# Optimization experiments

Hardware: AMD Instinct MI355X
Metric: run time of the kernel (lower is better)

The kernel has to match this reference:

```python
import jax, jax.numpy as jnp
import numpy as np

REF_SCALE = 5.0


def _forward_warp(im, flow):
    """Bilinear scatter-add (splat) forward warp.
    im: [B,C,H,W], flow: [B,H,W,2] in pixel units. Returns [B,C,H,W].
    A pixel contributes to its 4 bilinear neighbors only if the whole
    2x2 footprint is inside the image (matches the CUDA kernel).
    """
    B, C, H, W = im.shape
    xs = flow[..., 0] + jnp.arange(W, dtype=flow.dtype)            # [B,H,W]
    ys = flow[..., 1] + jnp.arange(H, dtype=flow.dtype)[:, None]   # [B,H,W]
    x0 = jnp.floor(xs); y0 = jnp.floor(ys)
    x1 = x0 + 1.0;      y1 = y0 + 1.0
    valid = (x0 >= 0) & (x1 <= W - 1) & (y0 >= 0) & (y1 <= H - 1)
    x0i = x0.astype(jnp.int32); y0i = y0.astype(jnp.int32)
    x1i = x1.astype(jnp.int32); y1i = y1.astype(jnp.int32)
    w_nw = (x1 - xs) * (y1 - ys)
    w_ne = (xs - x0) * (y1 - ys)
    w_sw = (x1 - xs) * (ys - y0)
    w_se = (xs - x0) * (ys - y0)

    def splat_one(im_b, idx_b, w_b):
        # im_b: [C,H,W], idx_b: [H,W] int32, w_b: [H,W]
        contrib = (im_b * w_b).reshape(C, -1).T                    # [HW, C]
        return jax.ops.segment_sum(contrib, idx_b.reshape(-1), num_segments=H * W)

    out = jnp.zeros((B, H * W, C), dtype=im.dtype)
    for w_c, yi, xi in ((w_nw, y0i, x0i), (w_ne, y0i, x1i),
                        (w_sw, y1i, x0i), (w_se, y1i, x1i)):
        idx = jnp.where(valid, yi * W + xi, 0)
        wv = jnp.where(valid, w_c, jnp.zeros_like(w_c))
        out = out + jax.vmap(splat_one)(im, idx, wv)
    return out.transpose(0, 2, 1).reshape(B, C, H, W)


def setup_inputs() -> dict:
    key = jax.random.key(0)
    k1, k2, k3 = jax.random.split(key, 3)
    B, C, H, W = 8, 3, 384, 1280
    x = jax.random.normal(k1, (B, C, H, W), dtype=jnp.float32)
    flow = jax.random.normal(k2, (B, 2, H, W), dtype=jnp.float32) * 20.0  # realistic px displacement
    depth = jax.random.uniform(k3, (B, 1, H, W), dtype=jnp.float32) * 80.0  # metric depth [0,80]
    return {"x": x, "flow": flow, "depth": depth}


def reference(x, flow, depth):
    B, C, H, W = x.shape
    flow = jnp.clip(flow, -2.0 * W, 2.0 * W)
    flow = jnp.transpose(flow, (0, 2, 3, 1))                       # [B,H,W,2]
    depth = jnp.clip(depth, 0.001, 80.0)
    depth_weight = jnp.exp(-(depth - 40.0) / REF_SCALE)            # [B,1,H,W]
    mask = jnp.ones_like(depth)
    # Fuse the three splats (depth_weight, x*depth_weight, mask) into one
    # warp over stacked channels -- identical math, one scatter pass.
    stacked = jnp.concatenate([depth_weight, x * depth_weight, mask], axis=1)  # [B, 1+C+1, H, W]
    warped = _forward_warp(stacked, flow)
    dw_flowed = warped[:, 0:1]
    xw_flowed = warped[:, 1:1 + C]
    mask_flowed = warped[:, 1 + C:2 + C]
    invalid = mask_flowed < 0.5                                    # [B,1,H,W]
    xw_flowed = jnp.where(invalid, jnp.zeros_like(xw_flowed), xw_flowed)
    return xw_flowed / jnp.maximum(dw_flowed, 1e-7)
```

## Files before the change

kernel.cpp:

```cpp
#include <hip/hip_runtime.h>
#include <hip/hip_fp16.h>
#include <math.h>

#define BB 8
#define CC 3
#define HH 384
#define WW 1280
#define HW (HH * WW)
#define NPIX (BB * HW)

#define TILE 32
#define TXN 40
#define TYN 12
#define TILES (TXN * TYN)
#define BINS (BB * TILES)

#define PPT 16
#define TPB 256
#define PPB (PPT * TPB)
#define NBLK ((NPIX + PPB - 1) / PPB)


#define HPAD 1280
#define CAPL 2048
#define RCH 8
#define LCAP 1280

__device__ __forceinline__ int enc_of(int idx, const float* __restrict__ flow) {
  int b = idx / HW;
  int p = idx - b * HW;
  int h = p / WW;
  int w = p - h * WW;
  float fx = flow[(b * 2 + 0) * HW + p];
  float fy = flow[(b * 2 + 1) * HW + p];
  fx = fminf(fmaxf(fx, -2560.0f), 2560.0f);
  fy = fminf(fmaxf(fy, -2560.0f), 2560.0f);
  float xs = fx + (float)w;
  float ys = fy + (float)h;
  float x0 = floorf(xs);
  float y0 = floorf(ys);
  if (!(x0 >= 0.0f && x0 <= (float)(WW - 2) && y0 >= 0.0f &&
        y0 <= (float)(HH - 2)))
    return -1;
  int x0i = (int)x0;
  int y0i = (int)y0;
  int enc = (b * TILES + (y0i >> 5) * TXN + (x0i >> 5));
  if ((x0i & 31) == 31) enc |= 1 << 22;
  if ((y0i & 31) == 31) enc |= 1 << 23;
  return enc;
}

__device__ inline void splat_direct(int b, int p, const float* __restrict__ x,
                                    const float* __restrict__ flow,
                                    const float* __restrict__ depth,
                                    float* __restrict__ xw_acc,
                                    float* __restrict__ dw_acc,
                                    float* __restrict__ mask_acc) {
  int h = p / WW;
  int w = p - h * WW;
  float fx = flow[(b * 2 + 0) * HW + p];
  float fy = flow[(b * 2 + 1) * HW + p];
  fx = fminf(fmaxf(fx, -2560.0f), 2560.0f);
  fy = fminf(fmaxf(fy, -2560.0f), 2560.0f);
  float xs = fx + (float)w;
  float ys = fy + (float)h;
  float x0 = floorf(xs);
  float y0 = floorf(ys);
  if (!(x0 >= 0.0f && x0 <= (float)(WW - 2) && y0 >= 0.0f &&
        y0 <= (float)(HH - 2)))
    return;
  int x0i = (int)x0;
  int y0i = (int)y0;
  float ax = xs - x0;
  float ay = ys - y0;
  float w_nw = (1.0f - ax) * (1.0f - ay);
  float w_ne = ax * (1.0f - ay);
  float w_sw = (1.0f - ax) * ay;
  float w_se = ax * ay;
  float d = depth[b * HW + p];
  d = fminf(fmaxf(d, 0.001f), 80.0f);
  float dw = expf(-(d - 40.0f) * 0.2f);
  float xv0 = x[(b * CC + 0) * HW + p] * dw;
  float xv1 = x[(b * CC + 1) * HW + p] * dw;
  float xv2 = x[(b * CC + 2) * HW + p] * dw;
  float* dwb = dw_acc + b * HW;
  float* mkb = mask_acc + b * HW;
  float* xb0 = xw_acc + (b * CC + 0) * HW;
  float* xb1 = xw_acc + (b * CC + 1) * HW;
  float* xb2 = xw_acc + (b * CC + 2) * HW;
  int i_nw = y0i * WW + x0i;
  int ci[4] = {i_nw, i_nw + 1, i_nw + WW, i_nw + WW + 1};
  float cw[4] = {w_nw, w_ne, w_sw, w_se};
  for (int c = 0; c < 4; ++c) {
    atomicAdd(dwb + ci[c], cw[c] * dw);
    atomicAdd(mkb + ci[c], cw[c]);
    atomicAdd(xb0 + ci[c], cw[c] * xv0);
    atomicAdd(xb1 + ci[c], cw[c] * xv1);
    atomicAdd(xb2 + ci[c], cw[c] * xv2);
  }
}

__global__ __launch_bounds__(256) void splat_kernel(
    const float* __restrict__ x, const float* __restrict__ flow,
    const float* __restrict__ depth, float* __restrict__ xw_acc,
    float* __restrict__ dw_acc, float* __restrict__ mask_acc) {
  int idx = blockIdx.x * blockDim.x + threadIdx.x;
  if (idx >= NPIX) return;
  int b = idx / HW;
  int p = idx - b * HW;
  splat_direct(b, p, x, flow, depth, xw_acc, dw_acc, mask_acc);
}

__global__ __launch_bounds__(256) void normalize_kernel(
    float* __restrict__ out, const float* __restrict__ dw_acc,
    const float* __restrict__ mask_acc) {
  int idx = blockIdx.x * blockDim.x + threadIdx.x;
  if (idx >= NPIX) return;
  int b = idx / HW;
  int p = idx - b * HW;
  float m = mask_acc[b * HW + p];
  float dwv = dw_acc[b * HW + p];
  float inv = 1.0f / fmaxf(dwv, 1e-7f);
  bool invalid = (m < 0.5f);
  float* ob = out + (b * CC) * HW + p;
  for (int c = 0; c < CC; ++c) {
    float xw = ob[c * HW];
    ob[c * HW] = invalid ? 0.0f : xw * inv;
  }
}

__global__ __launch_bounds__(TPB) void bin_fused_kernel(
    const float* __restrict__ x, const float* __restrict__ flow,
    const float* __restrict__ depth, unsigned int* __restrict__ counts,
    uint4* __restrict__ records, int cap) {
  __shared__ unsigned int cnt[BINS];
  int tid = threadIdx.x;
  int blk0 = blockIdx.x * PPB;

  for (int i = tid; i < BINS; i += TPB) cnt[i] = 0u;
  __syncthreads();

  int binr[PPT];
#pragma unroll
  for (int k = 0; k < PPT; ++k) {
    int idx = blk0 + k * TPB + tid;
    int enc = (idx < NPIX) ? enc_of(idx, flow) : -1;
    if (enc >= 0) {
      int bin = enc & 0xFFF;
      bool dE = (enc >> 22) & 1;
      bool dS = (enc >> 23) & 1;
      atomicAdd(&cnt[bin], 1u);
      if (dE) atomicAdd(&cnt[bin + 1], 1u);
      if (dS) atomicAdd(&cnt[bin + TXN], 1u);
      if (dE && dS) atomicAdd(&cnt[bin + TXN + 1], 1u);
    }
    binr[k] = enc;
  }
  __syncthreads();

  for (int i = tid; i < BINS; i += TPB) {
    unsigned int c = cnt[i];
    if (c) cnt[i] = atomicAdd(&counts[i], c);
  }
  __syncthreads();

#pragma unroll
  for (int k = 0; k < PPT; ++k) {
    int enc = binr[k];
    if (enc < 0) continue;
    int idx = blk0 + k * TPB + tid;
    int b = idx / HW;
    int p = idx - b * HW;
    int h = p / WW;
    int w = p - h * WW;
    float fx = flow[(b * 2 + 0) * HW + p];
    float fy = flow[(b * 2 + 1) * HW + p];
    fx = fminf(fmaxf(fx, -2560.0f), 2560.0f);
    fy = fminf(fmaxf(fy, -2560.0f), 2560.0f);
    float xs = fx + (float)w;
    float ys = fy + (float)h;
    float d = depth[b * HW + p];
    d = fminf(fmaxf(d, 0.001f), 80.0f);
    float dw = expf(-(d - 40.0f) * 0.2f);
    unsigned int dwh = (unsigned int)__half_as_ushort(__float2half(dw));
    unsigned int x0h = (unsigned int)__half_as_ushort(
        __float2half(x[(b * CC + 0) * HW + p]));
    unsigned int x1h = (unsigned int)__half_as_ushort(
        __float2half(x[(b * CC + 1) * HW + p]));
    unsigned int x2h = (unsigned int)__half_as_ushort(
        __float2half(x[(b * CC + 2) * HW + p]));
    uint4 rec = make_uint4(__float_as_uint(xs), __float_as_uint(ys),
                           x0h | (x1h << 16), x2h | (dwh << 16));
    int bin = enc & 0xFFF;
    bool dE = (enc >> 22) & 1;
    bool dS = (enc >> 23) & 1;

#define EMIT(BN)                                            \
    do {                                                    \
      int bn_ = (BN);                                       \
      unsigned int slot_ = atomicAdd(&cnt[bn_], 1u);        \
      if (slot_ < (unsigned int)cap)                        \
        records[(size_t)bn_ * cap + slot_] = rec;           \
    } while (0)

    EMIT(bin);
    if (dE) EMIT(bin + 1);
    if (dS) EMIT(bin + TXN);
    if (dE && dS) EMIT(bin + TXN + 1);
#undef EMIT
  }
}

__global__ __launch_bounds__(256) void tile_gather_kernel(
    const unsigned int* __restrict__ counts, const uint4* __restrict__ records,
    int cap, float* __restrict__ out) {
  __shared__ unsigned int hist[HPAD];
  __shared__ unsigned int tsum[256];
  __shared__ uint4 srec[LCAP];

  int bin = blockIdx.x;
  int b = bin / TILES;
  int t = bin - b * TILES;
  int ty = t / TXN;
  int tx = t - ty * TXN;
  int tid = threadIdx.x;
  int ox = tx * TILE;
  int oy = ty * TILE;

  for (int i = tid; i < HPAD; i += 256) hist[i] = 0u;
  __syncthreads();

  unsigned int n = counts[bin];
  if (n > (unsigned int)cap) n = (unsigned int)cap;
  const uint4* recbase = records + (size_t)bin * cap;

  uint4 rr[RCH];
  int kr[RCH];
#pragma unroll
  for (int c = 0; c < RCH; ++c) {
    unsigned int r = (unsigned int)tid + (unsigned int)c * 256u;
    int key = -1;
    if (r < n) {
      rr[c] = recbase[r];
      int x0i = (int)floorf(__uint_as_float(rr[c].x));
      int y0i = (int)floorf(__uint_as_float(rr[c].y));
      int sx = x0i - ox + 1;
      int sy = y0i - oy + 1;
      key = sy * 33 + sx;
      atomicAdd(&hist[key], 1u);
    }
    kr[c] = key;
  }
  __syncthreads();

  unsigned int loc[5];
  unsigned int s = 0;
#pragma unroll
  for (int j = 0; j < 5; ++j) {
    loc[j] = s;
    s += hist[tid * 5 + j];
  }
  tsum[tid] = s;
  __syncthreads();
  for (int d = 1; d < 256; d <<= 1) {
    unsigned int v = (tid >= d) ? tsum[tid - d] : 0u;
    __syncthreads();
    tsum[tid] += v;
    __syncthreads();
  }
  unsigned int bexcl = (tid == 0) ? 0u : tsum[tid - 1];
#pragma unroll
  for (int j = 0; j < 5; ++j) hist[tid * 5 + j] = bexcl + loc[j];
  __syncthreads();

  if (n <= LCAP) {
#pragma unroll
    for (int c = 0; c < RCH; ++c) {
      int key = kr[c];
      if (key >= 0) {
        unsigned int pos = atomicAdd(&hist[key], 1u);
        srec[pos] = rr[c];
      }
    }
    __syncthreads();

    int cy = (tid >> 3) + 1;
    int cx0 = (tid & 7) * 4 + 1;
    float aDw[4] = {0, 0, 0, 0}, aM[4] = {0, 0, 0, 0};
    float aX0[4] = {0, 0, 0, 0}, aX1[4] = {0, 0, 0, 0}, aX2[4] = {0, 0, 0, 0};
#pragma unroll
    for (int dy = 0; dy < 2; ++dy) {
      int sy = cy - 1 + dy;
      int kL = sy * 33 + cx0 - 1;
      int kR = kL + 4;
      unsigned int q0 = (kL == 0) ? 0u : hist[kL - 1];
      unsigned int q1 = hist[kR];
      for (unsigned int q = q0; q < q1; ++q) {
        uint4 w0 = srec[q];
        float xs = __uint_as_float(w0.x);
        float ys = __uint_as_float(w0.y);
        float fx0 = floorf(xs);
        float fy0 = floorf(ys);
        float ax = xs - fx0;
        float ay = ys - fy0;
        int sx = (int)fx0 - ox + 1;
        float wy = dy ? (1.0f - ay) : ay;
        float c0 = (1.0f - ax) * wy;
        float c1 = ax * wy;
        int j = sx - cx0;
        float dw = __half2float(__ushort_as_half((unsigned short)(w0.w >> 16)));
        float xv0 = __half2float(__ushort_as_half((unsigned short)(w0.z & 0xffffu)));
        float xv1 = __half2float(__ushort_as_half((unsigned short)(w0.z >> 16)));
        float xv2 = __half2float(__ushort_as_half((unsigned short)(w0.w & 0xffffu)));
        float xd0 = xv0 * dw, xd1 = xv1 * dw, xd2 = xv2 * dw;
#pragma unroll
        for (int jj = 0; jj < 4; ++jj) {
          float wc = (j == jj ? c0 : 0.0f) + (j + 1 == jj ? c1 : 0.0f);
          aDw[jj] += wc * dw;
          aM[jj] += wc;
          aX0[jj] += wc * xd0;
          aX1[jj] += wc * xd1;
          aX2[jj] += wc * xd2;
        }
      }
    }
    int gy = oy + cy - 1;
    int gx0 = ox + cx0 - 1;
#pragma unroll
    for (int jj = 0; jj < 4; ++jj) {
      float inv = 1.0f / fmaxf(aDw[jj], 1e-7f);
      bool invalid = (aM[jj] < 0.5f);
      int g = gy * WW + gx0 + jj;
      out[(b * CC + 0) * HW + g] = invalid ? 0.0f : aX0[jj] * inv;
      out[(b * CC + 1) * HW + g] = invalid ? 0.0f : aX1[jj] * inv;
      out[(b * CC + 2) * HW + g] = invalid ? 0.0f : aX2[jj] * inv;
    }
  } else {
    unsigned short* idx16 = (unsigned short*)srec;
#pragma unroll
    for (int c = 0; c < RCH; ++c) {
      int key = kr[c];
      if (key >= 0) {
        unsigned int r = (unsigned int)tid + (unsigned int)c * 256u;
        unsigned int pos = atomicAdd(&hist[key], 1u);
        idx16[pos] = (unsigned short)r;
      }
    }
    __syncthreads();

    for (int i = tid; i < TILE * TILE; i += 256) {
      int cy = (i >> 5) + 1;
      int cx = (i & 31) + 1;
      float aDw = 0.0f, aM = 0.0f, aX0 = 0.0f, aX1 = 0.0f, aX2 = 0.0f;
#pragma unroll
      for (int dy = 0; dy < 2; ++dy) {
        int sy = cy - 1 + dy;
        int k0 = sy * 33 + cx - 1;
        unsigned int q0 = (k0 == 0) ? 0u : hist[k0 - 1];
        unsigned int q1 = hist[k0 + 1];
        for (unsigned int q = q0; q < q1; ++q) {
          uint4 w0 = recbase[(int)idx16[q]];
          float xs = __uint_as_float(w0.x);
          float ys = __uint_as_float(w0.y);
          float fx0 = floorf(xs);
          float fy0 = floorf(ys);
          float ax = xs - fx0;
          float ay = ys - fy0;
          int sx = (int)fx0 - ox + 1;
          float wx = (sx == cx) ? (1.0f - ax) : ax;
          float wy = dy ? (1.0f - ay) : ay;
          float wgt = wx * wy;
          float dw = __half2float(__ushort_as_half((unsigned short)(w0.w >> 16)));
          float xv0 = __half2float(__ushort_as_half((unsigned short)(w0.z & 0xffffu)));
          float xv1 = __half2float(__ushort_as_half((unsigned short)(w0.z >> 16)));
          float xv2 = __half2float(__ushort_as_half((unsigned short)(w0.w & 0xffffu)));
          aDw += wgt * dw;
          aM += wgt;
          aX0 += wgt * (xv0 * dw);
          aX1 += wgt * (xv1 * dw);
          aX2 += wgt * (xv2 * dw);
        }
      }
      float inv = 1.0f / fmaxf(aDw, 1e-7f);
      bool invalid = (aM < 0.5f);
      int gy = oy + cy - 1;
      int gx = ox + cx - 1;
      int g = gy * WW + gx;
      out[(b * CC + 0) * HW + g] = invalid ? 0.0f : aX0 * inv;
      out[(b * CC + 1) * HW + g] = invalid ? 0.0f : aX1 * inv;
      out[(b * CC + 2) * HW + g] = invalid ? 0.0f : aX2 * inv;
    }
  }
}

extern "C" void kernel_launch(void* const* d_in, const int* in_sizes, int n_in,
                              void* d_out, int out_size, void* d_ws, size_t ws_size,
                              hipStream_t stream) {
  const float* x = (const float*)d_in[0];
  const float* flow = (const float*)d_in[1];
  const float* depth = (const float*)d_in[2];
  float* out = (float*)d_out;

  int n = NPIX;
  int blocks = (n + 255) / 256;

  {
    unsigned int* counts = (unsigned int*)d_ws;
    uint4* records = (uint4*)(counts + BINS);
    long long avail = (long long)ws_size - (long long)BINS * 4;
    int cap = avail > 0 ? (int)(avail / ((long long)BINS * 16)) : 0;
    if (cap > CAPL) cap = CAPL;
    if (cap >= 1400) {
      hipMemsetAsync(counts, 0, (size_t)BINS * sizeof(unsigned int), stream);
      bin_fused_kernel<<<NBLK, TPB, 0, stream>>>(x, flow, depth, counts,
                                                 records, cap);
      tile_gather_kernel<<<BINS, 256, 0, stream>>>(counts, records, cap, out);
      return;
    }
  }

  float* dw_acc = (float*)d_ws;
  float* mask_acc = dw_acc + (size_t)NPIX;
  hipMemsetAsync(d_out, 0, (size_t)BB * CC * HW * sizeof(float), stream);
  hipMemsetAsync(d_ws, 0, (size_t)2 * NPIX * sizeof(float), stream);
  splat_kernel<<<blocks, 256, 0, stream>>>(x, flow, depth, out, dw_acc,
                                           mask_acc);
  normalize_kernel<<<blocks, 256, 0, stream>>>(out, dw_acc, mask_acc);
}
```

Before: 90.42 us.

## Sort binned records in shared memory before writing coalesced to global bins

Replaces the binning kernel with one that computes the record once per pixel and keeps it in registers instead of re-reading flow. A block-wide prefix scan orders the records by bin in an LDS staging buffer, so they can then be written out contiguously. This targets the scattered 16-byte global writes. Pixels per thread drop from 16 to 8. The cost is heavy LDS use (about 60KB) that limits occupancy, plus extra barriers for the scan.

```diff
diff --git a/kernel.cpp b/kernel.cpp
--- a/kernel.cpp
+++ b/kernel.cpp
@@ -15,40 +15,18 @@
 #define TILES (TXN * TYN)
 #define BINS (BB * TILES)
 
-#define PPT 16
 #define TPB 256
-#define PPB (PPT * TPB)
-#define NBLK ((NPIX + PPB - 1) / PPB)
+
+#define PPT2 8
+#define PPB2 (PPT2 * TPB)
+#define NBLK2 (NPIX / PPB2)
+#define LBUF 2304
 
 
 #define HPAD 1280
 #define CAPL 2048
 #define RCH 8
 #define LCAP 1280
-
-__device__ __forceinline__ int enc_of(int idx, const float* __restrict__ flow) {
-  int b = idx / HW;
-  int p = idx - b * HW;
-  int h = p / WW;
-  int w = p - h * WW;
-  float fx = flow[(b * 2 + 0) * HW + p];
-  float fy = flow[(b * 2 + 1) * HW + p];
-  fx = fminf(fmaxf(fx, -2560.0f), 2560.0f);
-  fy = fminf(fmaxf(fy, -2560.0f), 2560.0f);
-  float xs = fx + (float)w;
-  float ys = fy + (float)h;
-  float x0 = floorf(xs);
-  float y0 = floorf(ys);
-  if (!(x0 >= 0.0f && x0 <= (float)(WW - 2) && y0 >= 0.0f &&
-        y0 <= (float)(HH - 2)))
-    return -1;
-  int x0i = (int)x0;
-  int y0i = (int)y0;
-  int enc = (b * TILES + (y0i >> 5) * TXN + (x0i >> 5));
-  if ((x0i & 31) == 31) enc |= 1 << 22;
-  if ((y0i & 31) == 31) enc |= 1 << 23;
-  return enc;
-}
 
 __device__ inline void splat_direct(int b, int p, const float* __restrict__ x,
                                     const float* __restrict__ flow,
@@ -129,45 +107,27 @@
   }
 }
 
-__global__ __launch_bounds__(TPB) void bin_fused_kernel(
+__global__ __launch_bounds__(TPB) void bin_sort_kernel(
     const float* __restrict__ x, const float* __restrict__ flow,
     const float* __restrict__ depth, unsigned int* __restrict__ counts,
     uint4* __restrict__ records, int cap) {
   __shared__ unsigned int cnt[BINS];
+  __shared__ unsigned int base[BINS];
+  __shared__ unsigned int tsum[256];
+  __shared__ uint4 srecL[LBUF];
+  __shared__ unsigned short sbin[LBUF];
+
   int tid = threadIdx.x;
-  int blk0 = blockIdx.x * PPB;
+  int blk0 = blockIdx.x * PPB2;
 
   for (int i = tid; i < BINS; i += TPB) cnt[i] = 0u;
   __syncthreads();
 
-  int binr[PPT];
-#pragma unroll
-  for (int k = 0; k < PPT; ++k) {
-    int idx = blk0 + k * TPB + tid;
-    int enc = (idx < NPIX) ? enc_of(idx, flow) : -1;
-    if (enc >= 0) {
-      int bin = enc & 0xFFF;
-      bool dE = (enc >> 22) & 1;
-      bool dS = (enc >> 23) & 1;
-      atomicAdd(&cnt[bin], 1u);
-      if (dE) atomicAdd(&cnt[bin + 1], 1u);
-      if (dS) atomicAdd(&cnt[bin + TXN], 1u);
-      if (dE && dS) atomicAdd(&cnt[bin + TXN + 1], 1u);
-    }
-    binr[k] = enc;
-  }
-  __syncthreads();
-
-  for (int i = tid; i < BINS; i += TPB) {
-    unsigned int c = cnt[i];
-    if (c) cnt[i] = atomicAdd(&counts[i], c);
-  }
-  __syncthreads();
-
-#pragma unroll
-  for (int k = 0; k < PPT; ++k) {
-    int enc = binr[k];
-    if (enc < 0) continue;
+  int binr[PPT2];
+  uint4 rr[PPT2];
+
+#pragma unroll
+  for (int k = 0; k < PPT2; ++k) {
     int idx = blk0 + k * TPB + tid;
     int b = idx / HW;
     int p = idx - b * HW;
@@ -179,28 +139,90 @@
     fy = fminf(fmaxf(fy, -2560.0f), 2560.0f);
     float xs = fx + (float)w;
     float ys = fy + (float)h;
-    float d = depth[b * HW + p];
-    d = fminf(fmaxf(d, 0.001f), 80.0f);
-    float dw = expf(-(d - 40.0f) * 0.2f);
-    unsigned int dwh = (unsigned int)__half_as_ushort(__float2half(dw));
-    unsigned int x0h = (unsigned int)__half_as_ushort(
-        __float2half(x[(b * CC + 0) * HW + p]));
-    unsigned int x1h = (unsigned int)__half_as_ushort(
-        __float2half(x[(b * CC + 1) * HW + p]));
-    unsigned int x2h = (unsigned int)__half_as_ushort(
-        __float2half(x[(b * CC + 2) * HW + p]));
-    uint4 rec = make_uint4(__float_as_uint(xs), __float_as_uint(ys),
-                           x0h | (x1h << 16), x2h | (dwh << 16));
+    float x0 = floorf(xs);
+    float y0 = floorf(ys);
+    int enc = -1;
+    rr[k] = make_uint4(0u, 0u, 0u, 0u);
+    if (x0 >= 0.0f && x0 <= (float)(WW - 2) && y0 >= 0.0f &&
+        y0 <= (float)(HH - 2)) {
+      int x0i = (int)x0;
+      int y0i = (int)y0;
+      enc = b * TILES + (y0i >> 5) * TXN + (x0i >> 5);
+      bool dE = ((x0i & 31) == 31);
+      bool dS = ((y0i & 31) == 31);
+      if (dE) enc |= 1 << 22;
+      if (dS) enc |= 1 << 23;
+      float d = depth[b * HW + p];
+      d = fminf(fmaxf(d, 0.001f), 80.0f);
+      float dw = expf(-(d - 40.0f) * 0.2f);
+      unsigned int dwh = (unsigned int)__half_as_ushort(__float2half(dw));
+      unsigned int x0h = (unsigned int)__half_as_ushort(
+          __float2half(x[(b * CC + 0) * HW + p]));
+      unsigned int x1h = (unsigned int)__half_as_ushort(
+          __float2half(x[(b * CC + 1) * HW + p]));
+      unsigned int x2h = (unsigned int)__half_as_ushort(
+          __float2half(x[(b * CC + 2) * HW + p]));
+      rr[k] = make_uint4(__float_as_uint(xs), __float_as_uint(ys),
+                         x0h | (x1h << 16), x2h | (dwh << 16));
+      int bin = enc & 0xFFF;
+      atomicAdd(&cnt[bin], 1u);
+      if (dE) atomicAdd(&cnt[bin + 1], 1u);
+      if (dS) atomicAdd(&cnt[bin + TXN], 1u);
+      if (dE && dS) atomicAdd(&cnt[bin + TXN + 1], 1u);
+    }
+    binr[k] = enc;
+  }
+  __syncthreads();
+
+  unsigned int loc[15];
+  unsigned int s = 0;
+#pragma unroll
+  for (int j = 0; j < 15; ++j) {
+    loc[j] = s;
+    s += cnt[tid * 15 + j];
+  }
+  tsum[tid] = s;
+  __syncthreads();
+  for (int d = 1; d < 256; d <<= 1) {
+    unsigned int v = (tid >= d) ? tsum[tid - d] : 0u;
+    __syncthreads();
+    tsum[tid] += v;
+    __syncthreads();
+  }
+  unsigned int bexcl = (tid == 0) ? 0u : tsum[tid - 1];
+#pragma unroll
+  for (int j = 0; j < 15; ++j) base[tid * 15 + j] = bexcl + loc[j];
+  __syncthreads();
+
+  for (int i = tid; i < BINS; i += TPB) {
+    unsigned int c = cnt[i];
+    if (c) {
+      unsigned int g = atomicAdd(&counts[i], c);
+      cnt[i] = g + (unsigned int)i * (unsigned int)cap - base[i];
+    }
+  }
+  __syncthreads();
+
+#pragma unroll
+  for (int k = 0; k < PPT2; ++k) {
+    int enc = binr[k];
+    if (enc < 0) continue;
     int bin = enc & 0xFFF;
     bool dE = (enc >> 22) & 1;
     bool dS = (enc >> 23) & 1;
 
-#define EMIT(BN)                                            \
-    do {                                                    \
-      int bn_ = (BN);                                       \
-      unsigned int slot_ = atomicAdd(&cnt[bn_], 1u);        \
-      if (slot_ < (unsigned int)cap)                        \
-        records[(size_t)bn_ * cap + slot_] = rec;           \
+#define EMIT(BN)                                                         \
+    do {                                                                 \
+      int bn_ = (BN);                                                    \
+      unsigned int slot_ = atomicAdd(&base[bn_], 1u);                    \
+      if (slot_ < LBUF) {                                                \
+        srecL[slot_] = rr[k];                                            \
+        sbin[slot_] = (unsigned short)bn_;                               \
+      } else {                                                           \
+        unsigned int g_ = cnt[bn_] + slot_;                              \
+        if (g_ < (unsigned int)(bn_ + 1) * (unsigned int)cap)            \
+          records[g_] = rr[k];                                           \
+      }                                                                  \
     } while (0)
 
     EMIT(bin);
@@ -208,6 +230,15 @@
     if (dS) EMIT(bin + TXN);
     if (dE && dS) EMIT(bin + TXN + 1);
 #undef EMIT
+  }
+  __syncthreads();
+
+  unsigned int total = tsum[255];
+  if (total > LBUF) total = LBUF;
+  for (unsigned int r = tid; r < total; r += TPB) {
+    unsigned int bin = (unsigned int)sbin[r];
+    unsigned int g = cnt[bin] + r;
+    if (g < (bin + 1u) * (unsigned int)cap) records[g] = srecL[r];
   }
 }
 
@@ -412,7 +443,7 @@
     if (cap > CAPL) cap = CAPL;
     if (cap >= 1400) {
       hipMemsetAsync(counts, 0, (size_t)BINS * sizeof(unsigned int), stream);
-      bin_fused_kernel<<<NBLK, TPB, 0, stream>>>(x, flow, depth, counts,
+      bin_sort_kernel<<<NBLK2, TPB, 0, stream>>>(x, flow, depth, counts,
                                                  records, cap);
       tile_gather_kernel<<<BINS, 256, 0, stream>>>(counts, records, cap, out);
       return;
```

Result: slower. 110.8 us (+22.5%).
